# Kernel tuning notes

Measured on AMD Instinct MI355X. Metric: run time of the kernel, lower is better.

The kernel has to match this reference:

```python
import jax, jax.numpy as jnp
import numpy as np

H = 64  # hidden dim
D_IN = 15  # per-step feature dim


def _gru_layer(x, Wih, Whh, bih, bhh):
    """torch-style GRU, batch_first. x: [M, T, D] -> [M, T, H]."""
    xp = x @ Wih.T + bih  # [M, T, 3H], precomputed input projections

    def step(h, xt):
        gh = h @ Whh.T + bhh
        xr, xz, xn = jnp.split(xt, 3, axis=-1)
        hr, hz, hn = jnp.split(gh, 3, axis=-1)
        r = jax.nn.sigmoid(xr + hr)
        z = jax.nn.sigmoid(xz + hz)
        n = jnp.tanh(xn + r * hn)
        h_new = (1.0 - z) * n + z * h
        return h_new, h_new

    h0 = jnp.zeros((x.shape[0], Whh.shape[1]), x.dtype)
    _, hs = jax.lax.scan(step, h0, jnp.swapaxes(xp, 0, 1))  # [T, M, H]
    return jnp.swapaxes(hs, 0, 1)


def setup_inputs() -> dict:
    key = jax.random.key(0)
    ks = jax.random.split(key, 16)
    N, B, T = 500, 32, 32
    s = 0.05
    return {
        "raw": jax.random.normal(ks[0], (N, B, T, D_IN), dtype=jnp.float32),
        # GRU layer 1 (input 15 -> 64)
        "gru1_Wih": jax.random.normal(ks[1], (3 * H, D_IN), dtype=jnp.float32) * s,
        "gru1_Whh": jax.random.normal(ks[2], (3 * H, H), dtype=jnp.float32) * s,
        "gru1_bih": jax.random.normal(ks[3], (3 * H,), dtype=jnp.float32) * s,
        "gru1_bhh": jax.random.normal(ks[4], (3 * H,), dtype=jnp.float32) * s,
        # GRU layer 2 (64 -> 64)
        "gru2_Wih": jax.random.normal(ks[5], (3 * H, H), dtype=jnp.float32) * s,
        "gru2_Whh": jax.random.normal(ks[6], (3 * H, H), dtype=jnp.float32) * s,
        "gru2_bih": jax.random.normal(ks[7], (3 * H,), dtype=jnp.float32) * s,
        "gru2_bhh": jax.random.normal(ks[8], (3 * H,), dtype=jnp.float32) * s,
        # temporal attention fc (64 -> 1)
        "attn_W": jax.random.normal(ks[9], (1, H), dtype=jnp.float32) * s,
        "attn_b": jax.random.normal(ks[10], (1,), dtype=jnp.float32) * s,
        # GAT attention-block linear W (64 -> 64) and u (128,)
        "gat_W_w": jax.random.normal(ks[11], (H, H), dtype=jnp.float32) * s,
        "gat_W_b": jax.random.normal(ks[12], (H,), dtype=jnp.float32) * s,
        "gat_u": jax.random.normal(ks[13], (2 * H,), dtype=jnp.float32) * s,
        # GAT value projection W1 (64 -> 64)
        "gat_W1_w": jax.random.normal(ks[14], (H, H), dtype=jnp.float32) * s,
        "gat_W1_b": jax.random.normal(ks[15], (H,), dtype=jnp.float32) * s,
    }


def reference(raw, gru1_Wih, gru1_Whh, gru1_bih, gru1_bhh,
              gru2_Wih, gru2_Whh, gru2_bih, gru2_bhh,
              attn_W, attn_b, gat_W_w, gat_W_b, gat_u, gat_W1_w, gat_W1_b):
    N, B, T, D = raw.shape
    x = raw.reshape(N * B, T, D)

    # SequenceEncoder: two stacked GRUs + temporal attention (dropout = eval identity)
    h = _gru_layer(x, gru1_Wih, gru1_Whh, gru1_bih, gru1_bhh)
    h = _gru_layer(h, gru2_Wih, gru2_Whh, gru2_bih, gru2_bhh)  # [NB, T, H]
    scores = jnp.tanh(h @ attn_W.T + attn_b)                    # [NB, T, 1]
    w = jax.nn.softmax(scores, axis=1)                          # softmax over time
    Ai = jnp.sum(h * w, axis=1).reshape(N, B, H)                # [N, B, H]

    # GAT over all-to-all node graph
    sq = Ai @ gat_W_w.T + gat_W_b          # attention-block projection [N, B, H]
    s_q = sq @ gat_u[:H]                   # query-side score [N, B]
    s_k = sq @ gat_u[H:]                   # neighbor-side score [N, B]
    score = s_q[:, None, :] + s_k[None, :, :]                   # [Nq, Nk, B]
    beta = jnp.exp(jax.nn.leaky_relu(score, negative_slope=0.01))
    beta = beta / jnp.sum(beta, axis=1, keepdims=True)          # normalize over neighbors
    proj = Ai @ gat_W1_w.T + gat_W1_b                           # value projection [N, B, H]
    g = jax.nn.relu(jnp.einsum('qkb,kbd->qbd', beta, proj))     # [N, B, H]
    return g
```

## Files before the change

### kernel.cpp

```cpp
#include <hip/hip_runtime.h>

#define TT 32
#define DIN 15
#define LOG2E 1.44269504088896340736f

typedef _Float16 f16x8 __attribute__((ext_vector_type(8)));
typedef _Float16 f16x4 __attribute__((ext_vector_type(4)));
typedef float f32x4 __attribute__((ext_vector_type(4)));

__device__ __forceinline__ float rcp_(float x){ return __builtin_amdgcn_rcpf(x); }
__device__ __forceinline__ float exp2_(float x){ return __builtin_amdgcn_exp2f(x); }
__device__ __forceinline__ float tanh_(float x){ return fmaf(-2.f, rcp_(__expf(2.f*x)+1.f), 1.f); }

#define MFMA(a,b,c) __builtin_amdgcn_mfma_f32_16x16x32_f16(a,b,c,0,0,0)

__device__ __forceinline__ f16x8 f16x8_zero(){
  f16x8 v;
  #pragma unroll
  for (int j=0;j<8;++j) v[j]=(_Float16)0.f;
  return v;
}

__global__ void wprep(const float* __restrict__ w1ih, const float* __restrict__ w1hh,
                      const float* __restrict__ w2ih, const float* __restrict__ w2hh,
                      const float* __restrict__ b1ih, const float* __restrict__ b1hh,
                      const float* __restrict__ W1,
                      const float* __restrict__ Ww, const float* __restrict__ Wb,
                      const float* __restrict__ u,
                      _Float16* __restrict__ wf, float* __restrict__ vqk){
  int id = blockIdx.x*256 + threadIdx.x;
  if (id < 47104){
    int e = id & 7, c = id >> 3;
    float v, scale;
    if (c < 4608){
      int mat = c / 1536; int r = c - mat*1536;
      int lane = r & 63, kf = (r>>6)&1, q = r>>7;
      const float* W = (mat==0)? w1hh : (mat==1)? w2ih : w2hh;
      int ht = q/3, g3 = q - ht*3;
      int row = g3*64 + ht*16 + (lane & 15);
      int k = kf*32 + (lane>>4)*8 + e;
      v = W[row*64 + k];
      scale = (g3==2) ? 2.f*LOG2E : -LOG2E;
    } else if (c < 5376){
      int r = c - 4608; int lane = r & 63, q = r>>6;
      int ht = q/3, g3 = q - ht*3;
      int row = g3*64 + ht*16 + (lane & 15);
      int k = (lane>>4)*8 + e;
      if (k < DIN)       v = w1ih[row*DIN + k];
      else if (k == DIN) v = (g3 < 2) ? (b1ih[row] + b1hh[row]) : b1ih[row];
      else               v = 0.f;
      scale = (g3==2) ? 2.f*LOG2E : -LOG2E;
    } else {
      int r = c - 5376; int lane = r & 63, q = r>>6;
      int ht = q>>1, kf = q&1;
      int row = ht*16 + (lane & 15);
      int k = kf*32 + (lane>>4)*8 + e;
      v = W1[row*64 + k]; scale = 1.f;
    }
    wf[c*8 + e] = (_Float16)(v*scale);
  } else if (id < 47104 + 130){
    int t = id - 47104;
    if (t < 128){
      int which = t>>6, j = t&63;
      float s = 0.f;
      for (int i=0;i<64;++i) s = fmaf(u[which*64+i], Ww[i*64+j], s);
      vqk[t] = s;
    } else {
      int which = t-128;
      float s = 0.f;
      for (int i=0;i<64;++i) s = fmaf(u[which*64+i], Wb[i], s);
      vqk[128+which] = s;
    }
  }
}

__global__ __launch_bounds__(256, 2) void gru_mfma(
    const float* __restrict__ raw,
    const _Float16* __restrict__ wf,
    const float* __restrict__ vqk,
    const float* __restrict__ bhh1,
    const float* __restrict__ bih2, const float* __restrict__ bhh2,
    const float* __restrict__ attnW, const float* __restrict__ attnb,
    const float* __restrict__ W1b,
    _Float16* __restrict__ projh, float* __restrict__ sqT, float* __restrict__ skT)
{
  __shared__ _Float16 xfh[TT*64*8];
  __shared__ _Float16 h1s[2][32*64];
  __shared__ _Float16 h2s[2][32*64];
  __shared__ float bias2[256];
  __shared__ float attp[2][2][4][16];
  __shared__ float attq[4][32], attk[4][32];

  const int tid  = threadIdx.x;
  const int lane = tid & 63;
  const int ht   = tid >> 6;
  const int g    = lane >> 4;
  const int sl   = lane & 15;
  const int s7   = sl & 7;
  const int n    = blockIdx.x;
  const int seq0 = n*32;
  const int row0 = ht*16 + g*4;

  { int* z2 = (int*)h2s[0]; for (int i=tid; i<1024; i+=256) z2[i]=0; }
  if (tid < 64){
    bias2[tid]       = -(bih2[tid]      + bhh2[tid])   *LOG2E;
    bias2[64+tid]    = -(bih2[64+tid]   + bhh2[64+tid])*LOG2E;
    bias2[128+tid]   =  bih2[128+tid]*(2.f*LOG2E);
    bias2[192+tid]   =  bhh2[128+tid]*(2.f*LOG2E);
  }
  for (int idx=tid; idx<TT*32; idx+=256){
    int s = idx & 31, t = idx >> 5;
    const float* rp = &raw[(size_t)(seq0+s)*(TT*DIN) + t*DIN];
    f16x8 lo, hi;
    #pragma unroll
    for (int j=0;j<8;++j){
      lo[j] = (_Float16)rp[j];
      hi[j] = (j<7) ? (_Float16)rp[8+j] : (_Float16)1.0f;
    }
    *(f16x8*)(xfh + ((size_t)t*64 +      s)*8) = lo;
    *(f16x8*)(xfh + ((size_t)t*64 + 32 + s)*8) = hi;
  }

  const f16x8* wf8 = (const f16x8*)wf;
  f16x8 wr1_0 = wf8[((ht*3+0)*2+0)*64 + lane], wr1_1 = wf8[((ht*3+0)*2+1)*64 + lane];
  f16x8 wz1_0 = wf8[((ht*3+1)*2+0)*64 + lane], wz1_1 = wf8[((ht*3+1)*2+1)*64 + lane];
  f16x8 wn1_0 = wf8[((ht*3+2)*2+0)*64 + lane], wn1_1 = wf8[((ht*3+2)*2+1)*64 + lane];
  f16x8 ar2_0 = wf8[1536+((ht*3+0)*2+0)*64 + lane], ar2_1 = wf8[1536+((ht*3+0)*2+1)*64 + lane];
  f16x8 az2_0 = wf8[1536+((ht*3+1)*2+0)*64 + lane], az2_1 = wf8[1536+((ht*3+1)*2+1)*64 + lane];
  f16x8 an2_0 = wf8[1536+((ht*3+2)*2+0)*64 + lane], an2_1 = wf8[1536+((ht*3+2)*2+1)*64 + lane];
  f16x8 br2_0 = wf8[3072+((ht*3+0)*2+0)*64 + lane], br2_1 = wf8[3072+((ht*3+0)*2+1)*64 + lane];
  f16x8 bz2_0 = wf8[3072+((ht*3+1)*2+0)*64 + lane], bz2_1 = wf8[3072+((ht*3+1)*2+1)*64 + lane];
  f16x8 bn2_0 = wf8[3072+((ht*3+2)*2+0)*64 + lane], bn2_1 = wf8[3072+((ht*3+2)*2+1)*64 + lane];
  f16x8 xr1 = wf8[4608 + (ht*3+0)*64 + lane];
  f16x8 xz1 = wf8[4608 + (ht*3+1)*64 + lane];
  f16x8 xn1 = wf8[4608 + (ht*3+2)*64 + lane];

  f32x4 Bhn1, awv;
  #pragma unroll
  for (int r=0;r<4;++r){ Bhn1[r] = bhh1[128+row0+r]*(2.f*LOG2E); awv[r] = attnW[row0+r]; }
  const float ab = attnb[0];

  __syncthreads();

  const f16x8 fz = f16x8_zero();
  f32x4 h1c0={0,0,0,0}, h1c1={0,0,0,0}, h2c0={0,0,0,0}, h2c1={0,0,0,0};
  f32x4 num0={0,0,0,0}, num1={0,0,0,0};
  float den0=0.f, den1=0.f;
  const int cwr = (((ht*2+(g>>1)) ^ s7))*8 + (g&1)*4;

  {
    f16x8 xf0 = fz, xf1 = fz;
    if (g < 2){
      xf0 = *(const f16x8*)(xfh + ((size_t)0*64 + g*32 +      sl)*8);
      xf1 = *(const f16x8*)(xfh + ((size_t)0*64 + g*32 + 16 + sl)*8);
    }
    f32x4 Cr0={0,0,0,0}, Cz0={0,0,0,0}, Cxn0={0,0,0,0}, Chn0=Bhn1;
    f32x4 Cr1={0,0,0,0}, Cz1={0,0,0,0}, Cxn1={0,0,0,0}, Chn1=Bhn1;
    Cr0 = MFMA(xr1,xf0,Cr0); Cz0 = MFMA(xz1,xf0,Cz0); Cxn0 = MFMA(xn1,xf0,Cxn0);
    Cr1 = MFMA(xr1,xf1,Cr1); Cz1 = MFMA(xz1,xf1,Cz1); Cxn1 = MFMA(xn1,xf1,Cxn1);
    f16x4 hw0, hw1;
    #pragma unroll
    for (int r=0;r<4;++r){
      float rg0 = rcp_(1.f + exp2_(Cr0[r]));
      float zg0 = rcp_(1.f + exp2_(Cz0[r]));
      float ng0 = fmaf(-2.f, rcp_(exp2_(Cxn0[r] + rg0*Chn0[r]) + 1.f), 1.f);
      float h0  = ng0 - zg0*ng0;
      h1c0[r] = h0; hw0[r] = (_Float16)h0;
      float rg1 = rcp_(1.f + exp2_(Cr1[r]));
      float zg1 = rcp_(1.f + exp2_(Cz1[r]));
      float ng1 = fmaf(-2.f, rcp_(exp2_(Cxn1[r] + rg1*Chn1[r]) + 1.f), 1.f);
      float h1v = ng1 - zg1*ng1;
      h1c1[r] = h1v; hw1[r] = (_Float16)h1v;
    }
    *(f16x4*)(h1s[0] + sl*64      + cwr) = hw0;
    *(f16x4*)(h1s[0] + (16+sl)*64 + cwr) = hw1;
  }
  __syncthreads();

  #pragma unroll 1
  for (int i=0; i<TT; ++i){
    const _Float16* h1rd = h1s[i&1];
    const _Float16* h2rd = h2s[i&1];
    _Float16* h1wr = h1s[(i+1)&1];
    _Float16* h2wr = h2s[(i+1)&1];
    f16x8 h1f0_0 = *(const f16x8*)(h1rd + sl*64      + ((g    ^s7))*8);
    f16x8 h1f0_1 = *(const f16x8*)(h1rd + sl*64      + (((4+g)^s7))*8);
    f16x8 h1f1_0 = *(const f16x8*)(h1rd + (16+sl)*64 + ((g    ^s7))*8);
    f16x8 h1f1_1 = *(const f16x8*)(h1rd + (16+sl)*64 + (((4+g)^s7))*8);
    f16x8 h2f0_0 = *(const f16x8*)(h2rd + sl*64      + ((g    ^s7))*8);
    f16x8 h2f0_1 = *(const f16x8*)(h2rd + sl*64      + (((4+g)^s7))*8);
    f16x8 h2f1_0 = *(const f16x8*)(h2rd + (16+sl)*64 + ((g    ^s7))*8);
    f16x8 h2f1_1 = *(const f16x8*)(h2rd + (16+sl)*64 + (((4+g)^s7))*8);
    const int tn = (i < TT-1) ? i+1 : TT-1;
    f16x8 xf0 = fz, xf1 = fz;
    if (g < 2){
      xf0 = *(const f16x8*)(xfh + ((size_t)tn*64 + g*32 +      sl)*8);
      xf1 = *(const f16x8*)(xfh + ((size_t)tn*64 + g*32 + 16 + sl)*8);
    }
    if (i > 0){
      const float (*ap)[4][16] = attp[(i+1)&1];
      float s40 = ap[0][0][sl]+ap[0][1][sl]+ap[0][2][sl]+ap[0][3][sl];
      float s41 = ap[1][0][sl]+ap[1][1][sl]+ap[1][2][sl]+ap[1][3][sl];
      float e0 = __expf(tanh_(s40 + ab));
      float e1 = __expf(tanh_(s41 + ab));
      den0 += e0; den1 += e1;
      #pragma unroll
      for (int r=0;r<4;++r){
        num0[r] = fmaf(e0, h2c0[r], num0[r]);
        num1[r] = fmaf(e1, h2c1[r], num1[r]);
      }
    }
    f32x4 Dr0  = *(const f32x4*)(bias2 + row0);
    f32x4 Dz0  = *(const f32x4*)(bias2 + 64 + row0);
    f32x4 Dxn0 = *(const f32x4*)(bias2 + 128 + row0);
    f32x4 Dhn0 = *(const f32x4*)(bias2 + 192 + row0);
    f32x4 Dr1 = Dr0, Dz1 = Dz0, Dxn1 = Dxn0, Dhn1 = Dhn0;
    Dr0  = MFMA(ar2_0,h1f0_0,Dr0);  Dr0  = MFMA(ar2_1,h1f0_1,Dr0);
    Dr0  = MFMA(br2_0,h2f0_0,Dr0);  Dr0  = MFMA(br2_1,h2f0_1,Dr0);
    Dr1  = MFMA(ar2_0,h1f1_0,Dr1);  Dr1  = MFMA(ar2_1,h1f1_1,Dr1);
    Dr1  = MFMA(br2_0,h2f1_0,Dr1);  Dr1  = MFMA(br2_1,h2f1_1,Dr1);
    Dz0  = MFMA(az2_0,h1f0_0,Dz0);  Dz0  = MFMA(az2_1,h1f0_1,Dz0);
    Dz0  = MFMA(bz2_0,h2f0_0,Dz0);  Dz0  = MFMA(bz2_1,h2f0_1,Dz0);
    Dz1  = MFMA(az2_0,h1f1_0,Dz1);  Dz1  = MFMA(az2_1,h1f1_1,Dz1);
    Dz1  = MFMA(bz2_0,h2f1_0,Dz1);  Dz1  = MFMA(bz2_1,h2f1_1,Dz1);
    Dxn0 = MFMA(an2_0,h1f0_0,Dxn0); Dxn0 = MFMA(an2_1,h1f0_1,Dxn0);
    Dxn1 = MFMA(an2_0,h1f1_0,Dxn1); Dxn1 = MFMA(an2_1,h1f1_1,Dxn1);
    Dhn0 = MFMA(bn2_0,h2f0_0,Dhn0); Dhn0 = MFMA(bn2_1,h2f0_1,Dhn0);
    Dhn1 = MFMA(bn2_0,h2f1_0,Dhn1); Dhn1 = MFMA(bn2_1,h2f1_1,Dhn1);
    f32x4 Cr0={0,0,0,0}, Cz0={0,0,0,0}, Cxn0={0,0,0,0}, Chn0=Bhn1;
    f32x4 Cr1={0,0,0,0}, Cz1={0,0,0,0}, Cxn1={0,0,0,0}, Chn1=Bhn1;
    Cr0 = MFMA(wr1_0,h1f0_0,Cr0); Cr0 = MFMA(wr1_1,h1f0_1,Cr0); Cr0 = MFMA(xr1,xf0,Cr0);
    Cr1 = MFMA(wr1_0,h1f1_0,Cr1); Cr1 = MFMA(wr1_1,h1f1_1,Cr1); Cr1 = MFMA(xr1,xf1,Cr1);
    Cz0 = MFMA(wz1_0,h1f0_0,Cz0); Cz0 = MFMA(wz1_1,h1f0_1,Cz0); Cz0 = MFMA(xz1,xf0,Cz0);
    Cz1 = MFMA(wz1_0,h1f1_0,Cz1); Cz1 = MFMA(wz1_1,h1f1_1,Cz1); Cz1 = MFMA(xz1,xf1,Cz1);
    Chn0 = MFMA(wn1_0,h1f0_0,Chn0); Chn0 = MFMA(wn1_1,h1f0_1,Chn0);
    Chn1 = MFMA(wn1_0,h1f1_0,Chn1); Chn1 = MFMA(wn1_1,h1f1_1,Chn1);
    Cxn0 = MFMA(xn1,xf0,Cxn0);
    Cxn1 = MFMA(xn1,xf1,Cxn1);
    f16x4 hw0, hw1;
    float p0 = 0.f, p1 = 0.f;
    #pragma unroll
    for (int r=0;r<4;++r){
      float rg0 = rcp_(1.f + exp2_(Dr0[r]));
      float zg0 = rcp_(1.f + exp2_(Dz0[r]));
      float ng0 = fmaf(-2.f, rcp_(exp2_(Dxn0[r] + rg0*Dhn0[r]) + 1.f), 1.f);
      float h0  = ng0 + zg0*(h2c0[r] - ng0);
      h2c0[r] = h0; hw0[r] = (_Float16)h0;
      p0 = fmaf(h0, awv[r], p0);
      float rg1 = rcp_(1.f + exp2_(Dr1[r]));
      float zg1 = rcp_(1.f + exp2_(Dz1[r]));
      float ng1 = fmaf(-2.f, rcp_(exp2_(Dxn1[r] + rg1*Dhn1[r]) + 1.f), 1.f);
      float h1v = ng1 + zg1*(h2c1[r] - ng1);
      h2c1[r] = h1v; hw1[r] = (_Float16)h1v;
      p1 = fmaf(h1v, awv[r], p1);
    }
    *(f16x4*)(h2wr + sl*64      + cwr) = hw0;
    *(f16x4*)(h2wr + (16+sl)*64 + cwr) = hw1;
    p0 += __shfl_xor(p0, 16, 64); p0 += __shfl_xor(p0, 32, 64);
    p1 += __shfl_xor(p1, 16, 64); p1 += __shfl_xor(p1, 32, 64);
    if (lane < 16){ attp[i&1][0][ht][sl] = p0; attp[i&1][1][ht][sl] = p1; }
    if (i < TT-1){
      #pragma unroll
      for (int r=0;r<4;++r){
        float rg0 = rcp_(1.f + exp2_(Cr0[r]));
        float zg0 = rcp_(1.f + exp2_(Cz0[r]));
        float ng0 = fmaf(-2.f, rcp_(exp2_(Cxn0[r] + rg0*Chn0[r]) + 1.f), 1.f);
        float h0  = ng0 + zg0*(h1c0[r] - ng0);
        h1c0[r] = h0; hw0[r] = (_Float16)h0;
        float rg1 = rcp_(1.f + exp2_(Cr1[r]));
        float zg1 = rcp_(1.f + exp2_(Cz1[r]));
        float ng1 = fmaf(-2.f, rcp_(exp2_(Cxn1[r] + rg1*Chn1[r]) + 1.f), 1.f);
        float h1v = ng1 + zg1*(h1c1[r] - ng1);
        h1c1[r] = h1v; hw1[r] = (_Float16)h1v;
      }
      *(f16x4*)(h1wr + sl*64      + cwr) = hw0;
      *(f16x4*)(h1wr + (16+sl)*64 + cwr) = hw1;
    }
    __syncthreads();
  }
  {
    const float (*ap)[4][16] = attp[1];
    float s40 = ap[0][0][sl]+ap[0][1][sl]+ap[0][2][sl]+ap[0][3][sl];
    float s41 = ap[1][0][sl]+ap[1][1][sl]+ap[1][2][sl]+ap[1][3][sl];
    float e0 = __expf(tanh_(s40 + ab));
    float e1 = __expf(tanh_(s41 + ab));
    den0 += e0; den1 += e1;
    #pragma unroll
    for (int r=0;r<4;++r){
      num0[r] = fmaf(e0, h2c0[r], num0[r]);
      num1[r] = fmaf(e1, h2c1[r], num1[r]);
    }
  }
  float rd0 = rcp_(den0), rd1 = rcp_(den1);
  f32x4 av0, av1;
  #pragma unroll
  for (int r=0;r<4;++r){ av0[r] = num0[r]*rd0; av1[r] = num1[r]*rd1; }
  {
    f32x4 vq4 = *(const f32x4*)&vqk[row0];
    f32x4 vk4 = *(const f32x4*)&vqk[64+row0];
    float pq0=0.f, pk0=0.f, pq1=0.f, pk1=0.f;
    #pragma unroll
    for (int r=0;r<4;++r){
      pq0 = fmaf(av0[r], vq4[r], pq0); pk0 = fmaf(av0[r], vk4[r], pk0);
      pq1 = fmaf(av1[r], vq4[r], pq1); pk1 = fmaf(av1[r], vk4[r], pk1);
    }
    pq0 += __shfl_xor(pq0,16,64); pq0 += __shfl_xor(pq0,32,64);
    pk0 += __shfl_xor(pk0,16,64); pk0 += __shfl_xor(pk0,32,64);
    pq1 += __shfl_xor(pq1,16,64); pq1 += __shfl_xor(pq1,32,64);
    pk1 += __shfl_xor(pk1,16,64); pk1 += __shfl_xor(pk1,32,64);
    if (lane < 16){
      attq[ht][sl] = pq0;    attk[ht][sl] = pk0;
      attq[ht][16+sl] = pq1; attk[ht][16+sl] = pk1;
    }
  }
  { f16x4 af0, af1;
    #pragma unroll
    for (int r=0;r<4;++r){ af0[r] = (_Float16)av0[r]; af1[r] = (_Float16)av1[r]; }
    *(f16x4*)(h1s[0] + sl*64      + cwr) = af0;
    *(f16x4*)(h1s[0] + (16+sl)*64 + cwr) = af1; }
  __syncthreads();
  if (tid < 32){
    float q4 = attq[0][tid]+attq[1][tid]+attq[2][tid]+attq[3][tid];
    float k4 = attk[0][tid]+attk[1][tid]+attk[2][tid]+attk[3][tid];
    sqT[tid*512 + n] = (q4 + vqk[128])*LOG2E;
    skT[tid*512 + n] = (k4 + vqk[129])*LOG2E;
  }
  {
    f16x8 a0 = wf8[5376 + (ht*2+0)*64 + lane];
    f16x8 a1 = wf8[5376 + (ht*2+1)*64 + lane];
    f16x8 b00 = *(const f16x8*)(h1s[0] + sl*64      + ((g    ^s7))*8);
    f16x8 b01 = *(const f16x8*)(h1s[0] + sl*64      + (((4+g)^s7))*8);
    f16x8 b10 = *(const f16x8*)(h1s[0] + (16+sl)*64 + ((g    ^s7))*8);
    f16x8 b11 = *(const f16x8*)(h1s[0] + (16+sl)*64 + (((4+g)^s7))*8);
    f32x4 P0 = *(const f32x4*)&W1b[row0];
    f32x4 P1 = P0;
    P0 = MFMA(a0,b00,P0); P0 = MFMA(a1,b01,P0);
    P1 = MFMA(a0,b10,P1); P1 = MFMA(a1,b11,P1);
    f16x4 pf0, pf1;
    #pragma unroll
    for (int r=0;r<4;++r){ pf0[r] = (_Float16)P0[r]; pf1[r] = (_Float16)P1[r]; }
    *(f16x4*)(projh + (size_t)(seq0+sl)*64    + row0) = pf0;
    *(f16x4*)(projh + (size_t)(seq0+16+sl)*64 + row0) = pf1;
  }
}

__global__ __launch_bounds__(256) void gat_agg(
    const _Float16* __restrict__ projh,
    const float* __restrict__ sqT, const float* __restrict__ skT,
    float* __restrict__ out)
{
  __shared__ _Float16 pT[64*64];
  __shared__ float sks[512];
  const int tid  = threadIdx.x;
  const int lane = tid & 63;
  const int wv   = tid >> 6;
  const int b    = blockIdx.x & 31;
  const int qt   = blockIdx.x >> 5;
  const int sl   = lane & 15, g = lane >> 4;
  const int myq  = qt*64 + wv*16 + sl;
  const float sq_l = (myq < 500) ? sqT[b*512 + myq] : -1e30f;
  for (int j = tid; j < 512; j += 256) sks[j] = (j < 500) ? skT[b*512 + j] : -1e30f;

  f32x4 acc[4] = {{0,0,0,0},{0,0,0,0},{0,0,0,0},{0,0,0,0}};
  float den_l = 0.f;
  const int kr = tid & 63, dgrp = tid >> 6;

  f16x8 pv0 = f16x8_zero(), pv1 = f16x8_zero();
  if (kr < 500){
    const f16x8* pp = (const f16x8*)(projh + ((size_t)kr*32 + b)*64 + dgrp*16);
    pv0 = pp[0]; pv1 = pp[1];
  }

  #pragma unroll 1
  for (int kc=0; kc<8; ++kc){
    __syncthreads();
    { char* base = (char*)pT;
      const int klo = (kr & 7) << 1, khi = kr >> 3;
      #pragma unroll
      for (int j=0;j<16;++j){
        int d = dgrp*16 + j;
        _Float16 v = (j<8) ? pv0[j] : pv1[j-8];
        *(_Float16*)(base + d*128 + (((khi ^ (d&7))) << 4) + klo) = v;
      } }
    __syncthreads();
    if (kc < 7){
      int node = (kc+1)*64 + kr;
      if (node < 500){
        const f16x8* pp = (const f16x8*)(projh + ((size_t)node*32 + b)*64 + dgrp*16);
        pv0 = pp[0]; pv1 = pp[1];
      } else { pv0 = f16x8_zero(); pv1 = f16x8_zero(); }
    }
    #pragma unroll
    for (int kc32=0; kc32<2; ++kc32){
      const int kb = kc*64 + kc32*32 + g*8;
      float4 skv0 = *(const float4*)&sks[kb];
      float4 skv1 = *(const float4*)&sks[kb+4];
      float s[8] = {sq_l+skv0.x, sq_l+skv0.y, sq_l+skv0.z, sq_l+skv0.w,
                    sq_l+skv1.x, sq_l+skv1.y, sq_l+skv1.z, sq_l+skv1.w};
      f16x8 bf;
      #pragma unroll
      for (int e=0;e<8;++e){
        float sc = fmaxf(s[e], 0.01f*s[e]);
        float ev = exp2_(sc);
        den_l += ev;
        bf[e] = (_Float16)ev;
      }
      const char* base = (const char*)pT;
      #pragma unroll
      for (int dt=0; dt<4; ++dt){
        f16x8 a = *(const f16x8*)(base + (dt*16 + sl)*128 + (((kc32*4 + g) ^ (sl&7)) << 4));
        acc[dt] = MFMA(a, bf, acc[dt]);
      }
    }
  }
  den_l += __shfl_xor(den_l, 16, 64);
  den_l += __shfl_xor(den_l, 32, 64);
  const float rd = rcp_(den_l);
  if (myq < 500){
    #pragma unroll
    for (int dt=0; dt<4; ++dt){
      f32x4 o;
      #pragma unroll
      for (int r=0;r<4;++r) o[r] = fmaxf(acc[dt][r]*rd, 0.f);
      *(f32x4*)&out[((size_t)myq*32 + b)*64 + dt*16 + g*4] = o;
    }
  }
}

extern "C" void kernel_launch(void* const* d_in, const int* in_sizes, int n_in,
                              void* d_out, int out_size, void* d_ws, size_t ws_size,
                              hipStream_t stream) {
  const float* raw   = (const float*)d_in[0];
  const float* w1ih  = (const float*)d_in[1];
  const float* w1hh  = (const float*)d_in[2];
  const float* b1ih  = (const float*)d_in[3];
  const float* b1hh  = (const float*)d_in[4];
  const float* w2ih  = (const float*)d_in[5];
  const float* w2hh  = (const float*)d_in[6];
  const float* b2ih  = (const float*)d_in[7];
  const float* b2hh  = (const float*)d_in[8];
  const float* attW  = (const float*)d_in[9];
  const float* attb  = (const float*)d_in[10];
  const float* gWw   = (const float*)d_in[11];
  const float* gWb   = (const float*)d_in[12];
  const float* gu    = (const float*)d_in[13];
  const float* gW1   = (const float*)d_in[14];
  const float* gW1b  = (const float*)d_in[15];
  float* outp = (float*)d_out;

  char* wsb = (char*)d_ws;
  _Float16* projh = (_Float16*)wsb;
  float*    sqT   = (float*)(wsb + 2048000);
  float*    skT   = (float*)(wsb + 2048000 + 65536);
  _Float16* wfh   = (_Float16*)(wsb + 2048000 + 131072);
  float*    vqk   = (float*)(wsb + 2048000 + 131072 + 94208);

  wprep<<<185, 256, 0, stream>>>(w1ih, w1hh, w2ih, w2hh, b1ih, b1hh,
                                 gW1, gWw, gWb, gu, wfh, vqk);
  gru_mfma<<<500, 256, 0, stream>>>(raw, wfh, vqk, b1hh, b2ih, b2hh,
                                    attW, attb, gW1b, projh, sqT, skT);
  gat_agg<<<256, 256, 0, stream>>>(projh, sqT, skT, outp);
}
```

Before: 92.24 us.

## Cut GRU register pressure to allow three blocks per CU

Drops the fp32 per-thread hidden-state copies (h1c/h2c) and instead reloads the previous hidden state as fp16 from shared memory. Streams the h1/h2 fragments from LDS just before each MFMA group instead of holding all eight live at once, and raises launch bounds to 3 blocks per CU. The goal is more concurrent blocks to hide latency in the serial recurrence. In exchange it adds LDS reads and rounds the recurrent state to fp16, which may lose accuracy.

```diff
diff --git a/kernel.cpp b/kernel.cpp
--- a/kernel.cpp
+++ b/kernel.cpp
@@ -74,7 +74,7 @@
   }
 }
 
-__global__ __launch_bounds__(256, 2) void gru_mfma(
+__global__ __launch_bounds__(256, 3) void gru_mfma(
     const float* __restrict__ raw,
     const _Float16* __restrict__ wf,
     const float* __restrict__ vqk,
@@ -100,6 +100,9 @@
   const int n    = blockIdx.x;
   const int seq0 = n*32;
   const int row0 = ht*16 + g*4;
+  const int cwr  = (((ht*2+(g>>1)) ^ s7))*8 + (g&1)*4;
+  const int oT0  = sl*64, oT1 = (16+sl)*64;
+  const int c0   = (g ^ s7)*8, c1 = ((4+g) ^ s7)*8;
 
   { int* z2 = (int*)h2s[0]; for (int i=tid; i<1024; i+=256) z2[i]=0; }
   if (tid < 64){
@@ -143,10 +146,8 @@
   __syncthreads();
 
   const f16x8 fz = f16x8_zero();
-  f32x4 h1c0={0,0,0,0}, h1c1={0,0,0,0}, h2c0={0,0,0,0}, h2c1={0,0,0,0};
   f32x4 num0={0,0,0,0}, num1={0,0,0,0};
   float den0=0.f, den1=0.f;
-  const int cwr = (((ht*2+(g>>1)) ^ s7))*8 + (g&1)*4;
 
   {
     f16x8 xf0 = fz, xf1 = fz;
@@ -154,8 +155,8 @@
       xf0 = *(const f16x8*)(xfh + ((size_t)0*64 + g*32 +      sl)*8);
       xf1 = *(const f16x8*)(xfh + ((size_t)0*64 + g*32 + 16 + sl)*8);
     }
-    f32x4 Cr0={0,0,0,0}, Cz0={0,0,0,0}, Cxn0={0,0,0,0}, Chn0=Bhn1;
-    f32x4 Cr1={0,0,0,0}, Cz1={0,0,0,0}, Cxn1={0,0,0,0}, Chn1=Bhn1;
+    f32x4 Cr0={0,0,0,0}, Cz0={0,0,0,0}, Cxn0={0,0,0,0};
+    f32x4 Cr1={0,0,0,0}, Cz1={0,0,0,0}, Cxn1={0,0,0,0};
     Cr0 = MFMA(xr1,xf0,Cr0); Cz0 = MFMA(xz1,xf0,Cz0); Cxn0 = MFMA(xn1,xf0,Cxn0);
     Cr1 = MFMA(xr1,xf1,Cr1); Cz1 = MFMA(xz1,xf1,Cz1); Cxn1 = MFMA(xn1,xf1,Cxn1);
     f16x4 hw0, hw1;
@@ -163,17 +164,15 @@
     for (int r=0;r<4;++r){
       float rg0 = rcp_(1.f + exp2_(Cr0[r]));
       float zg0 = rcp_(1.f + exp2_(Cz0[r]));
-      float ng0 = fmaf(-2.f, rcp_(exp2_(Cxn0[r] + rg0*Chn0[r]) + 1.f), 1.f);
-      float h0  = ng0 - zg0*ng0;
-      h1c0[r] = h0; hw0[r] = (_Float16)h0;
+      float ng0 = fmaf(-2.f, rcp_(exp2_(Cxn0[r] + rg0*Bhn1[r]) + 1.f), 1.f);
+      hw0[r] = (_Float16)(ng0 - zg0*ng0);
       float rg1 = rcp_(1.f + exp2_(Cr1[r]));
       float zg1 = rcp_(1.f + exp2_(Cz1[r]));
-      float ng1 = fmaf(-2.f, rcp_(exp2_(Cxn1[r] + rg1*Chn1[r]) + 1.f), 1.f);
-      float h1v = ng1 - zg1*ng1;
-      h1c1[r] = h1v; hw1[r] = (_Float16)h1v;
-    }
-    *(f16x4*)(h1s[0] + sl*64      + cwr) = hw0;
-    *(f16x4*)(h1s[0] + (16+sl)*64 + cwr) = hw1;
+      float ng1 = fmaf(-2.f, rcp_(exp2_(Cxn1[r] + rg1*Bhn1[r]) + 1.f), 1.f);
+      hw1[r] = (_Float16)(ng1 - zg1*ng1);
+    }
+    *(f16x4*)(h1s[0] + oT0 + cwr) = hw0;
+    *(f16x4*)(h1s[0] + oT1 + cwr) = hw1;
   }
   __syncthreads();
 
@@ -183,20 +182,8 @@
     const _Float16* h2rd = h2s[i&1];
     _Float16* h1wr = h1s[(i+1)&1];
     _Float16* h2wr = h2s[(i+1)&1];
-    f16x8 h1f0_0 = *(const f16x8*)(h1rd + sl*64      + ((g    ^s7))*8);
-    f16x8 h1f0_1 = *(const f16x8*)(h1rd + sl*64      + (((4+g)^s7))*8);
-    f16x8 h1f1_0 = *(const f16x8*)(h1rd + (16+sl)*64 + ((g    ^s7))*8);
-    f16x8 h1f1_1 = *(const f16x8*)(h1rd + (16+sl)*64 + (((4+g)^s7))*8);
-    f16x8 h2f0_0 = *(const f16x8*)(h2rd + sl*64      + ((g    ^s7))*8);
-    f16x8 h2f0_1 = *(const f16x8*)(h2rd + sl*64      + (((4+g)^s7))*8);
-    f16x8 h2f1_0 = *(const f16x8*)(h2rd + (16+sl)*64 + ((g    ^s7))*8);
-    f16x8 h2f1_1 = *(const f16x8*)(h2rd + (16+sl)*64 + (((4+g)^s7))*8);
-    const int tn = (i < TT-1) ? i+1 : TT-1;
-    f16x8 xf0 = fz, xf1 = fz;
-    if (g < 2){
-      xf0 = *(const f16x8*)(xfh + ((size_t)tn*64 + g*32 +      sl)*8);
-      xf1 = *(const f16x8*)(xfh + ((size_t)tn*64 + g*32 + 16 + sl)*8);
-    }
+    f16x4 ho20 = *(const f16x4*)(h2rd + oT0 + cwr);
+    f16x4 ho21 = *(const f16x4*)(h2rd + oT1 + cwr);
     if (i > 0){
       const float (*ap)[4][16] = attp[(i+1)&1];
       float s40 = ap[0][0][sl]+ap[0][1][sl]+ap[0][2][sl]+ap[0][3][sl];
@@ -206,8 +193,8 @@
       den0 += e0; den1 += e1;
       #pragma unroll
       for (int r=0;r<4;++r){
-        num0[r] = fmaf(e0, h2c0[r], num0[r]);
-        num1[r] = fmaf(e1, h2c1[r], num1[r]);
+        num0[r] = fmaf(e0, (float)ho20[r], num0[r]);
+        num1[r] = fmaf(e1, (float)ho21[r], num1[r]);
       }
     }
     f32x4 Dr0  = *(const f32x4*)(bias2 + row0);
@@ -215,70 +202,97 @@
     f32x4 Dxn0 = *(const f32x4*)(bias2 + 128 + row0);
     f32x4 Dhn0 = *(const f32x4*)(bias2 + 192 + row0);
     f32x4 Dr1 = Dr0, Dz1 = Dz0, Dxn1 = Dxn0, Dhn1 = Dhn0;
-    Dr0  = MFMA(ar2_0,h1f0_0,Dr0);  Dr0  = MFMA(ar2_1,h1f0_1,Dr0);
-    Dr0  = MFMA(br2_0,h2f0_0,Dr0);  Dr0  = MFMA(br2_1,h2f0_1,Dr0);
-    Dr1  = MFMA(ar2_0,h1f1_0,Dr1);  Dr1  = MFMA(ar2_1,h1f1_1,Dr1);
-    Dr1  = MFMA(br2_0,h2f1_0,Dr1);  Dr1  = MFMA(br2_1,h2f1_1,Dr1);
-    Dz0  = MFMA(az2_0,h1f0_0,Dz0);  Dz0  = MFMA(az2_1,h1f0_1,Dz0);
-    Dz0  = MFMA(bz2_0,h2f0_0,Dz0);  Dz0  = MFMA(bz2_1,h2f0_1,Dz0);
-    Dz1  = MFMA(az2_0,h1f1_0,Dz1);  Dz1  = MFMA(az2_1,h1f1_1,Dz1);
-    Dz1  = MFMA(bz2_0,h2f1_0,Dz1);  Dz1  = MFMA(bz2_1,h2f1_1,Dz1);
-    Dxn0 = MFMA(an2_0,h1f0_0,Dxn0); Dxn0 = MFMA(an2_1,h1f0_1,Dxn0);
-    Dxn1 = MFMA(an2_0,h1f1_0,Dxn1); Dxn1 = MFMA(an2_1,h1f1_1,Dxn1);
-    Dhn0 = MFMA(bn2_0,h2f0_0,Dhn0); Dhn0 = MFMA(bn2_1,h2f0_1,Dhn0);
-    Dhn1 = MFMA(bn2_0,h2f1_0,Dhn1); Dhn1 = MFMA(bn2_1,h2f1_1,Dhn1);
-    f32x4 Cr0={0,0,0,0}, Cz0={0,0,0,0}, Cxn0={0,0,0,0}, Chn0=Bhn1;
-    f32x4 Cr1={0,0,0,0}, Cz1={0,0,0,0}, Cxn1={0,0,0,0}, Chn1=Bhn1;
-    Cr0 = MFMA(wr1_0,h1f0_0,Cr0); Cr0 = MFMA(wr1_1,h1f0_1,Cr0); Cr0 = MFMA(xr1,xf0,Cr0);
-    Cr1 = MFMA(wr1_0,h1f1_0,Cr1); Cr1 = MFMA(wr1_1,h1f1_1,Cr1); Cr1 = MFMA(xr1,xf1,Cr1);
-    Cz0 = MFMA(wz1_0,h1f0_0,Cz0); Cz0 = MFMA(wz1_1,h1f0_1,Cz0); Cz0 = MFMA(xz1,xf0,Cz0);
-    Cz1 = MFMA(wz1_0,h1f1_0,Cz1); Cz1 = MFMA(wz1_1,h1f1_1,Cz1); Cz1 = MFMA(xz1,xf1,Cz1);
-    Chn0 = MFMA(wn1_0,h1f0_0,Chn0); Chn0 = MFMA(wn1_1,h1f0_1,Chn0);
-    Chn1 = MFMA(wn1_0,h1f1_0,Chn1); Chn1 = MFMA(wn1_1,h1f1_1,Chn1);
-    Cxn0 = MFMA(xn1,xf0,Cxn0);
-    Cxn1 = MFMA(xn1,xf1,Cxn1);
-    f16x4 hw0, hw1;
-    float p0 = 0.f, p1 = 0.f;
-    #pragma unroll
-    for (int r=0;r<4;++r){
-      float rg0 = rcp_(1.f + exp2_(Dr0[r]));
-      float zg0 = rcp_(1.f + exp2_(Dz0[r]));
-      float ng0 = fmaf(-2.f, rcp_(exp2_(Dxn0[r] + rg0*Dhn0[r]) + 1.f), 1.f);
-      float h0  = ng0 + zg0*(h2c0[r] - ng0);
-      h2c0[r] = h0; hw0[r] = (_Float16)h0;
-      p0 = fmaf(h0, awv[r], p0);
-      float rg1 = rcp_(1.f + exp2_(Dr1[r]));
-      float zg1 = rcp_(1.f + exp2_(Dz1[r]));
-      float ng1 = fmaf(-2.f, rcp_(exp2_(Dxn1[r] + rg1*Dhn1[r]) + 1.f), 1.f);
-      float h1v = ng1 + zg1*(h2c1[r] - ng1);
-      h2c1[r] = h1v; hw1[r] = (_Float16)h1v;
-      p1 = fmaf(h1v, awv[r], p1);
-    }
-    *(f16x4*)(h2wr + sl*64      + cwr) = hw0;
-    *(f16x4*)(h2wr + (16+sl)*64 + cwr) = hw1;
-    p0 += __shfl_xor(p0, 16, 64); p0 += __shfl_xor(p0, 32, 64);
-    p1 += __shfl_xor(p1, 16, 64); p1 += __shfl_xor(p1, 32, 64);
-    if (lane < 16){ attp[i&1][0][ht][sl] = p0; attp[i&1][1][ht][sl] = p1; }
+    {
+      f16x8 p0 = *(const f16x8*)(h1rd + oT0 + c0);
+      f16x8 p1 = *(const f16x8*)(h1rd + oT1 + c0);
+      Dr0  = MFMA(ar2_0,p0,Dr0);  Dr1  = MFMA(ar2_0,p1,Dr1);
+      Dz0  = MFMA(az2_0,p0,Dz0);  Dz1  = MFMA(az2_0,p1,Dz1);
+      Dxn0 = MFMA(an2_0,p0,Dxn0); Dxn1 = MFMA(an2_0,p1,Dxn1);
+      p0 = *(const f16x8*)(h1rd + oT0 + c1);
+      p1 = *(const f16x8*)(h1rd + oT1 + c1);
+      Dr0  = MFMA(ar2_1,p0,Dr0);  Dr1  = MFMA(ar2_1,p1,Dr1);
+      Dz0  = MFMA(az2_1,p0,Dz0);  Dz1  = MFMA(az2_1,p1,Dz1);
+      Dxn0 = MFMA(an2_1,p0,Dxn0); Dxn1 = MFMA(an2_1,p1,Dxn1);
+      p0 = *(const f16x8*)(h2rd + oT0 + c0);
+      p1 = *(const f16x8*)(h2rd + oT1 + c0);
+      Dr0  = MFMA(br2_0,p0,Dr0);  Dr1  = MFMA(br2_0,p1,Dr1);
+      Dz0  = MFMA(bz2_0,p0,Dz0);  Dz1  = MFMA(bz2_0,p1,Dz1);
+      Dhn0 = MFMA(bn2_0,p0,Dhn0); Dhn1 = MFMA(bn2_0,p1,Dhn1);
+      p0 = *(const f16x8*)(h2rd + oT0 + c1);
+      p1 = *(const f16x8*)(h2rd + oT1 + c1);
+      Dr0  = MFMA(br2_1,p0,Dr0);  Dr1  = MFMA(br2_1,p1,Dr1);
+      Dz0  = MFMA(bz2_1,p0,Dz0);  Dz1  = MFMA(bz2_1,p1,Dz1);
+      Dhn0 = MFMA(bn2_1,p0,Dhn0); Dhn1 = MFMA(bn2_1,p1,Dhn1);
+    }
+    {
+      f16x4 hw0, hw1;
+      float p0 = 0.f, p1 = 0.f;
+      #pragma unroll
+      for (int r=0;r<4;++r){
+        float rg0 = rcp_(1.f + exp2_(Dr0[r]));
+        float zg0 = rcp_(1.f + exp2_(Dz0[r]));
+        float ng0 = fmaf(-2.f, rcp_(exp2_(Dxn0[r] + rg0*Dhn0[r]) + 1.f), 1.f);
+        float h0  = ng0 + zg0*((float)ho20[r] - ng0);
+        hw0[r] = (_Float16)h0; p0 = fmaf(h0, awv[r], p0);
+        float rg1 = rcp_(1.f + exp2_(Dr1[r]));
+        float zg1 = rcp_(1.f + exp2_(Dz1[r]));
+        float ng1 = fmaf(-2.f, rcp_(exp2_(Dxn1[r] + rg1*Dhn1[r]) + 1.f), 1.f);
+        float h1v = ng1 + zg1*((float)ho21[r] - ng1);
+        hw1[r] = (_Float16)h1v; p1 = fmaf(h1v, awv[r], p1);
+      }
+      *(f16x4*)(h2wr + oT0 + cwr) = hw0;
+      *(f16x4*)(h2wr + oT1 + cwr) = hw1;
+      p0 += __shfl_xor(p0, 16, 64); p0 += __shfl_xor(p0, 32, 64);
+      p1 += __shfl_xor(p1, 16, 64); p1 += __shfl_xor(p1, 32, 64);
+      if (lane < 16){ attp[i&1][0][ht][sl] = p0; attp[i&1][1][ht][sl] = p1; }
+    }
     if (i < TT-1){
+      f16x8 xf0 = fz, xf1 = fz;
+      if (g < 2){
+        xf0 = *(const f16x8*)(xfh + ((size_t)(i+1)*64 + g*32 +      sl)*8);
+        xf1 = *(const f16x8*)(xfh + ((size_t)(i+1)*64 + g*32 + 16 + sl)*8);
+      }
+      f32x4 Cr0={0,0,0,0}, Cz0={0,0,0,0}, Cxn0={0,0,0,0}, Chn0=Bhn1;
+      f32x4 Cr1={0,0,0,0}, Cz1={0,0,0,0}, Cxn1={0,0,0,0}, Chn1=Bhn1;
+      {
+        f16x8 p0 = *(const f16x8*)(h1rd + oT0 + c0);
+        f16x8 p1 = *(const f16x8*)(h1rd + oT1 + c0);
+        Cr0  = MFMA(wr1_0,p0,Cr0);  Cr1  = MFMA(wr1_0,p1,Cr1);
+        Cz0  = MFMA(wz1_0,p0,Cz0);  Cz1  = MFMA(wz1_0,p1,Cz1);
+        Chn0 = MFMA(wn1_0,p0,Chn0); Chn1 = MFMA(wn1_0,p1,Chn1);
+        p0 = *(const f16x8*)(h1rd + oT0 + c1);
+        p1 = *(const f16x8*)(h1rd + oT1 + c1);
+        Cr0  = MFMA(wr1_1,p0,Cr0);  Cr1  = MFMA(wr1_1,p1,Cr1);
+        Cz0  = MFMA(wz1_1,p0,Cz0);  Cz1  = MFMA(wz1_1,p1,Cz1);
+        Chn0 = MFMA(wn1_1,p0,Chn0); Chn1 = MFMA(wn1_1,p1,Chn1);
+      }
+      Cr0  = MFMA(xr1,xf0,Cr0);  Cr1  = MFMA(xr1,xf1,Cr1);
+      Cz0  = MFMA(xz1,xf0,Cz0);  Cz1  = MFMA(xz1,xf1,Cz1);
+      Cxn0 = MFMA(xn1,xf0,Cxn0); Cxn1 = MFMA(xn1,xf1,Cxn1);
+      f16x4 ho10 = *(const f16x4*)(h1rd + oT0 + cwr);
+      f16x4 ho11 = *(const f16x4*)(h1rd + oT1 + cwr);
+      f16x4 hw0, hw1;
       #pragma unroll
       for (int r=0;r<4;++r){
         float rg0 = rcp_(1.f + exp2_(Cr0[r]));
         float zg0 = rcp_(1.f + exp2_(Cz0[r]));
         float ng0 = fmaf(-2.f, rcp_(exp2_(Cxn0[r] + rg0*Chn0[r]) + 1.f), 1.f);
-        float h0  = ng0 + zg0*(h1c0[r] - ng0);
-        h1c0[r] = h0; hw0[r] = (_Float16)h0;
+        float h0  = ng0 + zg0*((float)ho10[r] - ng0);
+        hw0[r] = (_Float16)h0;
         float rg1 = rcp_(1.f + exp2_(Cr1[r]));
         float zg1 = rcp_(1.f + exp2_(Cz1[r]));
         float ng1 = fmaf(-2.f, rcp_(exp2_(Cxn1[r] + rg1*Chn1[r]) + 1.f), 1.f);
-        float h1v = ng1 + zg1*(h1c1[r] - ng1);
-        h1c1[r] = h1v; hw1[r] = (_Float16)h1v;
-      }
-      *(f16x4*)(h1wr + sl*64      + cwr) = hw0;
-      *(f16x4*)(h1wr + (16+sl)*64 + cwr) = hw1;
+        float h1v = ng1 + zg1*((float)ho11[r] - ng1);
+        hw1[r] = (_Float16)h1v;
+      }
+      *(f16x4*)(h1wr + oT0 + cwr) = hw0;
+      *(f16x4*)(h1wr + oT1 + cwr) = hw1;
     }
     __syncthreads();
   }
   {
+    f16x4 ho20 = *(const f16x4*)(h2s[0] + oT0 + cwr);
+    f16x4 ho21 = *(const f16x4*)(h2s[0] + oT1 + cwr);
     const float (*ap)[4][16] = attp[1];
     float s40 = ap[0][0][sl]+ap[0][1][sl]+ap[0][2][sl]+ap[0][3][sl];
     float s41 = ap[1][0][sl]+ap[1][1][sl]+ap[1][2][sl]+ap[1][3][sl];
@@ -287,8 +301,8 @@
     den0 += e0; den1 += e1;
     #pragma unroll
     for (int r=0;r<4;++r){
-      num0[r] = fmaf(e0, h2c0[r], num0[r]);
-      num1[r] = fmaf(e1, h2c1[r], num1[r]);
+      num0[r] = fmaf(e0, (float)ho20[r], num0[r]);
+      num1[r] = fmaf(e1, (float)ho21[r], num1[r]);
     }
   }
   float rd0 = rcp_(den0), rd1 = rcp_(den1);
@@ -316,8 +330,8 @@
   { f16x4 af0, af1;
     #pragma unroll
     for (int r=0;r<4;++r){ af0[r] = (_Float16)av0[r]; af1[r] = (_Float16)av1[r]; }
-    *(f16x4*)(h1s[0] + sl*64      + cwr) = af0;
-    *(f16x4*)(h1s[0] + (16+sl)*64 + cwr) = af1; }
+    *(f16x4*)(h1s[0] + oT0 + cwr) = af0;
+    *(f16x4*)(h1s[0] + oT1 + cwr) = af1; }
   __syncthreads();
   if (tid < 32){
     float q4 = attq[0][tid]+attq[1][tid]+attq[2][tid]+attq[3][tid];
@@ -328,10 +342,10 @@
   {
     f16x8 a0 = wf8[5376 + (ht*2+0)*64 + lane];
     f16x8 a1 = wf8[5376 + (ht*2+1)*64 + lane];
-    f16x8 b00 = *(const f16x8*)(h1s[0] + sl*64      + ((g    ^s7))*8);
-    f16x8 b01 = *(const f16x8*)(h1s[0] + sl*64      + (((4+g)^s7))*8);
-    f16x8 b10 = *(const f16x8*)(h1s[0] + (16+sl)*64 + ((g    ^s7))*8);
-    f16x8 b11 = *(const f16x8*)(h1s[0] + (16+sl)*64 + (((4+g)^s7))*8);
+    f16x8 b00 = *(const f16x8*)(h1s[0] + oT0 + c0);
+    f16x8 b01 = *(const f16x8*)(h1s[0] + oT0 + c1);
+    f16x8 b10 = *(const f16x8*)(h1s[0] + oT1 + c0);
+    f16x8 b11 = *(const f16x8*)(h1s[0] + oT1 + c1);
     f32x4 P0 = *(const f32x4*)&W1b[row0];
     f32x4 P1 = P0;
     P0 = MFMA(a0,b00,P0); P0 = MFMA(a1,b01,P0);
```

Result: slower. 120.8 us (+31.0%).
